# Optimization experiments

Measured on AMD Instinct MI355X. Metric: run time of the kernel, lower is better.

Reference implementation:

```python
import jax, jax.numpy as jnp
import numpy as np

B, S, E, H = 4, 2048, 1024, 16
DK = E // H  # 64


def setup_inputs() -> dict:
    key = jax.random.key(0)
    ks = jax.random.split(key, 6)
    scale = 1.0 / np.sqrt(E)
    return {
        "x": jax.random.normal(ks[0], (B, S, E), dtype=jnp.float32),
        "Wq": jax.random.normal(ks[1], (E, E), dtype=jnp.float32) * scale,
        "Wk": jax.random.normal(ks[2], (E, E), dtype=jnp.float32) * scale,
        "Wv": jax.random.normal(ks[3], (E, E), dtype=jnp.float32) * scale,
        "Wo": jax.random.normal(ks[4], (E, E), dtype=jnp.float32) * scale,
        "theta": jax.random.normal(ks[5], (DK,), dtype=jnp.float32),
    }


def _heads(t):
    # [B,S,E] -> [B,H,S,DK]
    b, s, _ = t.shape
    return t.reshape(b, s, H, DK).transpose(0, 2, 1, 3)


def reference(x, Wq, Wk, Wv, Wo, theta):
    # nn.Linear (no bias): y = x @ W.T
    # quantum transform: independent single-qubit RX(x)->RX(theta)->  <Z> = cos(x+theta)
    q = jnp.cos(_heads(x @ Wq.T) + theta)  # [B,H,S,DK]
    k = jnp.cos(_heads(x @ Wk.T) + theta)
    v = jnp.cos(_heads(x @ Wv.T) + theta)
    scores = jnp.einsum("bhqd,bhkd->bhqk", q, k) / jnp.sqrt(jnp.float32(DK))
    attn = jax.nn.softmax(scores, axis=-1)  # dropout is identity in eval
    out = jnp.einsum("bhqk,bhkd->bhqd", attn, v)  # [B,H,S,DK]
    out = out.transpose(0, 2, 1, 3).reshape(x.shape[0], -1, E)
    return out @ Wo.T
```

## Files before the change

kernel.cpp:

```cpp
#include <hip/hip_runtime.h>

#define B_  4
#define S_  2048
#define E_  1024
#define H_  16
#define DK_ 64
#define M_  (B_*S_)

typedef __attribute__((ext_vector_type(8)))  short short8;
typedef __attribute__((ext_vector_type(4)))  float f32x4;
typedef __attribute__((ext_vector_type(16))) float f32x16;

#define QSCALE 0.18033688f

__device__ __forceinline__ unsigned short f2b(float f) {
    union { float f; unsigned u; } v; v.f = f;
    unsigned u = v.u;
    return (unsigned short)((u + 0x7fffu + ((u >> 16) & 1u)) >> 16);
}

__device__ __forceinline__ void gload_lds16(const unsigned short* g, unsigned short* l) {
    __builtin_amdgcn_global_load_lds((const __attribute__((address_space(1))) void*)g,
                                     (__attribute__((address_space(3))) void*)l, 16, 0, 0);
}

#define XN4 (M_*E_/4)
#define WN4 (E_*E_/4)
__global__ __launch_bounds__(256) void cvt_all(
    const float* __restrict__ x,
    const float* __restrict__ w0, const float* __restrict__ w1,
    const float* __restrict__ w2, const float* __restrict__ w3,
    unsigned short* __restrict__ xb, unsigned short* __restrict__ wb,
    unsigned short* __restrict__ wob) {
    int i = blockIdx.x * 256 + threadIdx.x;
    const float* src;
    unsigned short* dst;
    int idx;
    if (i < XN4) { src = x; dst = xb; idx = i; }
    else {
        int j = i - XN4;
        int z = j >> 18;
        idx = j & (WN4 - 1);
        src = (z == 0) ? w0 : (z == 1) ? w1 : (z == 2) ? w2 : w3;
        dst = (z < 3) ? wb + (size_t)z * E_ * E_ : wob;
    }
    float4 f = ((const float4*)src)[idx];
    ushort4 o;
    o.x = f2b(f.x); o.y = f2b(f.y); o.z = f2b(f.z); o.w = f2b(f.w);
    ((ushort4*)dst)[idx] = o;
}

__global__ __launch_bounds__(256) void gemm_qkv(
    const unsigned short* __restrict__ xb,
    const unsigned short* __restrict__ Wb,
    const float* __restrict__ theta,
    unsigned short* __restrict__ qb,
    unsigned short* __restrict__ kb,
    unsigned short* __restrict__ vtb)
{
    __shared__ unsigned short smem[128*144];
    unsigned short* As = smem;
    unsigned short* Bs = smem + 128*64;
    const int tid = threadIdx.x;
    const int w = tid >> 6, lane = tid & 63, quad = lane >> 4, col = lane & 15;
    const int wm = (w & 1) * 64, wn = (w >> 1) * 64;
    const int m0 = blockIdx.x * 128, n0 = blockIdx.y * 128, z = blockIdx.z;
    const unsigned short* Wz = Wb + (size_t)z * E_ * E_;
    const int srow = lane >> 3;
    const int sch  = ((lane & 7) ^ srow) * 8;
    const int rsw  = col & 7;

    f32x4 acc[4][4] = {};
    for (int k0 = 0; k0 < E_; k0 += 64) {
        #pragma unroll
        for (int c = 0; c < 4; c++) {
            int row = w*32 + c*8 + srow;
            gload_lds16(&xb[(size_t)(m0+row)*E_ + k0 + sch], &As[(w*32 + c*8)*64]);
            gload_lds16(&Wz[(size_t)(n0+row)*E_ + k0 + sch], &Bs[(w*32 + c*8)*64]);
        }
        __syncthreads();
        #pragma unroll
        for (int kk = 0; kk < 64; kk += 32) {
            short8 a[4], b[4];
            #pragma unroll
            for (int i = 0; i < 4; i++)
                a[i] = *(const short8*)&As[(wm + i*16 + col)*64 + ((((kk>>3) + quad) ^ rsw) * 8)];
            #pragma unroll
            for (int j = 0; j < 4; j++)
                b[j] = *(const short8*)&Bs[(wn + j*16 + col)*64 + ((((kk>>3) + quad) ^ rsw) * 8)];
            #pragma unroll
            for (int i = 0; i < 4; i++)
                #pragma unroll
                for (int j = 0; j < 4; j++)
                    acc[i][j] = __builtin_amdgcn_mfma_f32_16x16x32_bf16(a[i], b[j], acc[i][j], 0, 0, 0);
        }
        __syncthreads();
    }

    const int bblk = m0 >> 11;
    const int sbase = m0 & (S_-1);

    if (z != 2) {
        const float qs = (z == 0) ? QSCALE : 1.0f;
        #pragma unroll
        for (int j = 0; j < 4; j++) {
            int nl = wn + j*16 + col;
            float th = theta[(n0 + nl) & 63];
            #pragma unroll
            for (int i = 0; i < 4; i++)
                #pragma unroll
                for (int r = 0; r < 4; r++) {
                    int ml = wm + i*16 + quad*4 + r;
                    int nls = nl ^ (((ml >> 2) & 3) << 4);
                    smem[ml*144 + nls] = f2b(__cosf(acc[i][j][r] + th) * qs);
                }
        }
        __syncthreads();
        unsigned short* dst = (z == 0) ? qb : kb;
        const int h0 = n0 >> 6;
        #pragma unroll
        for (int k = 0; k < 8; k++) {
            int idx = k*256 + tid;
            int chunk = idx & 7, seg = idx >> 3;
            int ml = seg >> 1, hh = seg & 1;
            int ch = chunk ^ (((ml >> 2) & 3) << 1);
            int4 val = *(const int4*)&smem[ml*144 + hh*64 + ch*8];
            size_t g = ((size_t)(bblk*H_ + h0 + hh)*S_ + sbase + ml)*DK_ + chunk*8;
            *(int4*)&dst[g] = val;
        }
    } else {
        #pragma unroll
        for (int j = 0; j < 4; j++) {
            int nl = wn + j*16 + col;
            float th = theta[(n0 + nl) & 63];
            #pragma unroll
            for (int i = 0; i < 4; i++)
                #pragma unroll
                for (int r = 0; r < 4; r++)
                    smem[nl*136 + wm + i*16 + quad*4 + r] = f2b(__cosf(acc[i][j][r] + th));
        }
        __syncthreads();
        int row = tid >> 1, halfm = (tid & 1) * 64;
        int n = n0 + row, h = n >> 6, d = n & 63;
        size_t base = ((size_t)(bblk*H_ + h)*DK_ + d)*S_ + sbase + halfm;
        #pragma unroll
        for (int k = 0; k < 8; k++)
            *(int4*)&vtb[base + k*8] = *(const int4*)&smem[row*136 + halfm + k*8];
    }
}

__global__ __launch_bounds__(256) void gemm_out(
    const unsigned short* __restrict__ ctx,
    const unsigned short* __restrict__ Wob,
    float* __restrict__ out)
{
    __shared__ unsigned short As[128*64];
    __shared__ unsigned short Bs[128*64];
    const int tid = threadIdx.x;
    const int w = tid >> 6, lane = tid & 63, quad = lane >> 4, col = lane & 15;
    const int wm = (w & 1) * 64, wn = (w >> 1) * 64;
    const int m0 = blockIdx.x * 128, n0 = blockIdx.y * 128;
    const int srow = lane >> 3;
    const int sch  = ((lane & 7) ^ srow) * 8;
    const int rsw  = col & 7;

    f32x4 acc[4][4] = {};
    for (int k0 = 0; k0 < E_; k0 += 64) {
        #pragma unroll
        for (int c = 0; c < 4; c++) {
            int row = w*32 + c*8 + srow;
            gload_lds16(&ctx[(size_t)(m0+row)*E_ + k0 + sch], &As[(w*32 + c*8)*64]);
            gload_lds16(&Wob[(size_t)(n0+row)*E_ + k0 + sch], &Bs[(w*32 + c*8)*64]);
        }
        __syncthreads();
        #pragma unroll
        for (int kk = 0; kk < 64; kk += 32) {
            short8 a[4], b[4];
            #pragma unroll
            for (int i = 0; i < 4; i++)
                a[i] = *(const short8*)&As[(wm + i*16 + col)*64 + ((((kk>>3) + quad) ^ rsw) * 8)];
            #pragma unroll
            for (int j = 0; j < 4; j++)
                b[j] = *(const short8*)&Bs[(wn + j*16 + col)*64 + ((((kk>>3) + quad) ^ rsw) * 8)];
            #pragma unroll
            for (int i = 0; i < 4; i++)
                #pragma unroll
                for (int j = 0; j < 4; j++)
                    acc[i][j] = __builtin_amdgcn_mfma_f32_16x16x32_bf16(a[i], b[j], acc[i][j], 0, 0, 0);
        }
        __syncthreads();
    }
    #pragma unroll
    for (int j = 0; j < 4; j++) {
        int n = n0 + wn + j*16 + col;
        #pragma unroll
        for (int i = 0; i < 4; i++)
            #pragma unroll
            for (int r = 0; r < 4; r++) {
                int m = m0 + wm + i*16 + quad*4 + r;
                out[(size_t)m*E_ + n] = acc[i][j][r];
            }
    }
}

#define LPK 72

__global__ __launch_bounds__(256, 4) void flash_attn(
    const unsigned short* __restrict__ qb,
    const unsigned short* __restrict__ kb,
    const unsigned short* __restrict__ vtb,
    unsigned short* __restrict__ ctx)
{
    __shared__ unsigned short Kt[2][64*LPK];
    __shared__ unsigned short Vt[2][64*LPK];
    const int tid = threadIdx.x;
    const int w = tid >> 6, lane = tid & 63, col = lane & 31, half = lane >> 5;

    const int f   = blockIdx.y * gridDim.x + blockIdx.x;
    const int swz = (f & 7) * 128 + (f >> 3);
    const int q0  = (swz & 15) * 128;
    const int bh  = swz >> 4;

    const unsigned short* kbase = kb  + (size_t)bh * S_ * DK_;
    const unsigned short* vbase = vtb + (size_t)bh * DK_ * S_;
    const int srow = tid >> 3;
    const int sc8  = (tid & 7) * 8;

    short8 qf[4];
    {
        const unsigned short* qrow = qb + ((size_t)bh*S_ + q0 + w*32 + col)*DK_;
        #pragma unroll
        for (int c = 0; c < 4; c++)
            qf[c] = *(const short8*)&qrow[c*16 + half*8];
    }

    union U8 { unsigned u[4]; short8 s8; };
    U8 ones;
    #pragma unroll
    for (int i = 0; i < 4; i++) ones.u[i] = 0x3F803F80u;

    f32x16 oacc[2] = {};
    f32x16 lacc = {};

    #pragma unroll
    for (int u = 0; u < 2; u++) {
        *(int4*)&Kt[0][(srow + u*32)*LPK + sc8] =
            *(const int4*)&kbase[(size_t)(srow + u*32)*DK_ + sc8];
        *(int4*)&Vt[0][(srow + u*32)*LPK + sc8] =
            *(const int4*)&vbase[(size_t)(srow + u*32)*S_ + sc8];
    }
    __syncthreads();

    for (int it = 0; it < S_/64; ++it) {
        const int cur = it & 1, nxt = cur ^ 1;
        const int ktn = it*64 + 64;
        int4 rk[2], rv[2];
        if (ktn < S_) {
            #pragma unroll
            for (int u = 0; u < 2; u++) {
                rk[u] = *(const int4*)&kbase[(size_t)(ktn + srow + u*32)*DK_ + sc8];
                rv[u] = *(const int4*)&vbase[(size_t)(srow + u*32)*S_ + ktn + sc8];
            }
        }

        #pragma unroll
        for (int t = 0; t < 2; t++) {
            f32x16 sacc = {};
            __builtin_amdgcn_s_setprio(1);
            #pragma unroll
            for (int c = 0; c < 4; c++) {
                short8 kf = *(const short8*)&Kt[cur][(t*32 + col)*LPK + c*16 + half*8];
                sacc = __builtin_amdgcn_mfma_f32_32x32x16_bf16(kf, qf[c], sacc, 0, 0, 0);
            }
            __builtin_amdgcn_s_setprio(0);
            unsigned pk[4][2];
            #pragma unroll
            for (int rg = 0; rg < 4; rg++) {
                float p0 = __builtin_amdgcn_exp2f(sacc[rg*4+0]);
                float p1 = __builtin_amdgcn_exp2f(sacc[rg*4+1]);
                float p2 = __builtin_amdgcn_exp2f(sacc[rg*4+2]);
                float p3 = __builtin_amdgcn_exp2f(sacc[rg*4+3]);
                pk[rg][0] = __builtin_amdgcn_perm(__float_as_uint(p1), __float_as_uint(p0), 0x07060302u);
                pk[rg][1] = __builtin_amdgcn_perm(__float_as_uint(p3), __float_as_uint(p2), 0x07060302u);
            }
            #pragma unroll
            for (int kc = 0; kc < 2; kc++) {
                const int lo = 2*kc, hi = 2*kc + 1;
                auto s0 = __builtin_amdgcn_permlane32_swap((int)pk[lo][0], (int)pk[hi][0], false, false);
                auto s1 = __builtin_amdgcn_permlane32_swap((int)pk[lo][1], (int)pk[hi][1], false, false);
                U8 pa;
                pa.u[0] = (unsigned)s0[0];
                pa.u[1] = (unsigned)s1[0];
                pa.u[2] = (unsigned)s0[1];
                pa.u[3] = (unsigned)s1[1];
                __builtin_amdgcn_s_setprio(1);
                lacc = __builtin_amdgcn_mfma_f32_32x32x16_bf16(pa.s8, ones.s8, lacc, 0, 0, 0);
                #pragma unroll
                for (int dt = 0; dt < 2; dt++) {
                    short8 vf = *(const short8*)&Vt[cur][(dt*32 + col)*LPK + t*32 + kc*16 + half*8];
                    oacc[dt] = __builtin_amdgcn_mfma_f32_32x32x16_bf16(pa.s8, vf, oacc[dt], 0, 0, 0);
                }
                __builtin_amdgcn_s_setprio(0);
            }
        }

        if (ktn < S_) {
            #pragma unroll
            for (int u = 0; u < 2; u++) {
                *(int4*)&Kt[nxt][(srow + u*32)*LPK + sc8] = rk[u];
                *(int4*)&Vt[nxt][(srow + u*32)*LPK + sc8] = rv[u];
            }
        }
        __syncthreads();
    }

    const int b = bh >> 4, h = bh & 15;
    #pragma unroll
    for (int rg = 0; rg < 4; rg++)
        #pragma unroll
        for (int rr = 0; rr < 4; rr++) {
            int row = rr + rg*8 + half*4;
            float inv = 1.0f / lacc[rg*4 + rr];
            int s = q0 + w*32 + row;
            size_t rowoff = ((size_t)(b*S_ + s))*E_ + h*64;
            #pragma unroll
            for (int dt = 0; dt < 2; dt++)
                ctx[rowoff + dt*32 + col] = f2b(oacc[dt][rg*4 + rr] * inv);
        }
}

extern "C" void kernel_launch(void* const* d_in, const int* in_sizes, int n_in,
                              void* d_out, int out_size, void* d_ws, size_t ws_size,
                              hipStream_t stream) {
    (void)in_sizes; (void)n_in; (void)out_size; (void)ws_size;
    const float* x     = (const float*)d_in[0];
    const float* Wq    = (const float*)d_in[1];
    const float* Wk    = (const float*)d_in[2];
    const float* Wv    = (const float*)d_in[3];
    const float* Wo    = (const float*)d_in[4];
    const float* theta = (const float*)d_in[5];
    float* out = (float*)d_out;

    unsigned short* ws  = (unsigned short*)d_ws;
    unsigned short* xb  = ws;
    unsigned short* Wb  = xb  + (size_t)M_*E_;
    unsigned short* Wob = Wb  + (size_t)3*E_*E_;
    unsigned short* qb  = Wob + (size_t)E_*E_;
    unsigned short* kb  = qb  + (size_t)B_*H_*S_*DK_;
    unsigned short* vtb = kb  + (size_t)B_*H_*S_*DK_;
    unsigned short* ctx = xb;

    cvt_all<<<(XN4 + 4*WN4)/256, 256, 0, stream>>>(x, Wq, Wk, Wv, Wo, xb, Wb, Wob);

    gemm_qkv<<<dim3(M_/128, E_/128, 3), 256, 0, stream>>>(xb, Wb, theta, qb, kb, vtb);
    flash_attn<<<dim3(S_/128, B_*H_), 256, 0, stream>>>(qb, kb, vtb, ctx);
    gemm_out<<<dim3(M_/128, E_/128), 256, 0, stream>>>(ctx, Wob, out);
}
```

Measured before the change: 281.9 us.

## Double query rows per warp in flash attention to reuse K/V fragments

Each warp now processes 64 query rows (two 32-row sub-tiles) instead of 32, so the block covers 256 queries and the grid halves. Each K and V fragment read from LDS now feeds two MFMAs, which halves LDS traffic and K/V global loads per query. In exchange, accumulator registers double, launch bounds drop to 2 blocks per CU, and the grid shrinks to 512 blocks, which lowers occupancy and the ability to hide latency.

```diff
diff --git a/kernel.cpp b/kernel.cpp
--- a/kernel.cpp
+++ b/kernel.cpp
@@ -205,7 +205,7 @@
 
 #define LPK 72
 
-__global__ __launch_bounds__(256, 4) void flash_attn(
+__global__ __launch_bounds__(256, 2) void flash_attn(
     const unsigned short* __restrict__ qb,
     const unsigned short* __restrict__ kb,
     const unsigned short* __restrict__ vtb,
@@ -217,21 +217,23 @@
     const int w = tid >> 6, lane = tid & 63, col = lane & 31, half = lane >> 5;
 
     const int f   = blockIdx.y * gridDim.x + blockIdx.x;
-    const int swz = (f & 7) * 128 + (f >> 3);
-    const int q0  = (swz & 15) * 128;
-    const int bh  = swz >> 4;
+    const int swz = (f & 7) * 64 + (f >> 3);
+    const int q0  = (swz & 7) * 256;
+    const int bh  = swz >> 3;
 
     const unsigned short* kbase = kb  + (size_t)bh * S_ * DK_;
     const unsigned short* vbase = vtb + (size_t)bh * DK_ * S_;
     const int srow = tid >> 3;
     const int sc8  = (tid & 7) * 8;
 
-    short8 qf[4];
+    short8 qf[2][4];
     {
-        const unsigned short* qrow = qb + ((size_t)bh*S_ + q0 + w*32 + col)*DK_;
-        #pragma unroll
-        for (int c = 0; c < 4; c++)
-            qf[c] = *(const short8*)&qrow[c*16 + half*8];
+        const unsigned short* qrow = qb + ((size_t)bh*S_ + q0 + w*64 + col)*DK_;
+        #pragma unroll
+        for (int s = 0; s < 2; s++)
+            #pragma unroll
+            for (int c = 0; c < 4; c++)
+                qf[s][c] = *(const short8*)&qrow[(size_t)s*32*DK_ + c*16 + half*8];
     }
 
     union U8 { unsigned u[4]; short8 s8; };
@@ -239,8 +241,8 @@
     #pragma unroll
     for (int i = 0; i < 4; i++) ones.u[i] = 0x3F803F80u;
 
-    f32x16 oacc[2] = {};
-    f32x16 lacc = {};
+    f32x16 oacc[2][2] = {};
+    f32x16 lacc[2] = {};
 
     #pragma unroll
     for (int u = 0; u < 2; u++) {
@@ -265,40 +267,52 @@
 
         #pragma unroll
         for (int t = 0; t < 2; t++) {
-            f32x16 sacc = {};
+            f32x16 sa0 = {}, sa1 = {};
             __builtin_amdgcn_s_setprio(1);
             #pragma unroll
             for (int c = 0; c < 4; c++) {
                 short8 kf = *(const short8*)&Kt[cur][(t*32 + col)*LPK + c*16 + half*8];
-                sacc = __builtin_amdgcn_mfma_f32_32x32x16_bf16(kf, qf[c], sacc, 0, 0, 0);
+                sa0 = __builtin_amdgcn_mfma_f32_32x32x16_bf16(kf, qf[0][c], sa0, 0, 0, 0);
+                sa1 = __builtin_amdgcn_mfma_f32_32x32x16_bf16(kf, qf[1][c], sa1, 0, 0, 0);
             }
             __builtin_amdgcn_s_setprio(0);
-            unsigned pk[4][2];
+            unsigned pk[2][4][2];
             #pragma unroll
             for (int rg = 0; rg < 4; rg++) {
-                float p0 = __builtin_amdgcn_exp2f(sacc[rg*4+0]);
-                float p1 = __builtin_amdgcn_exp2f(sacc[rg*4+1]);
-                float p2 = __builtin_amdgcn_exp2f(sacc[rg*4+2]);
-                float p3 = __builtin_amdgcn_exp2f(sacc[rg*4+3]);
-                pk[rg][0] = __builtin_amdgcn_perm(__float_as_uint(p1), __float_as_uint(p0), 0x07060302u);
-                pk[rg][1] = __builtin_amdgcn_perm(__float_as_uint(p3), __float_as_uint(p2), 0x07060302u);
+                float a0 = __builtin_amdgcn_exp2f(sa0[rg*4+0]);
+                float a1 = __builtin_amdgcn_exp2f(sa0[rg*4+1]);
+                float a2 = __builtin_amdgcn_exp2f(sa0[rg*4+2]);
+                float a3 = __builtin_amdgcn_exp2f(sa0[rg*4+3]);
+                pk[0][rg][0] = __builtin_amdgcn_perm(__float_as_uint(a1), __float_as_uint(a0), 0x07060302u);
+                pk[0][rg][1] = __builtin_amdgcn_perm(__float_as_uint(a3), __float_as_uint(a2), 0x07060302u);
+                float b0 = __builtin_amdgcn_exp2f(sa1[rg*4+0]);
+                float b1 = __builtin_amdgcn_exp2f(sa1[rg*4+1]);
+                float b2 = __builtin_amdgcn_exp2f(sa1[rg*4+2]);
+                float b3 = __builtin_amdgcn_exp2f(sa1[rg*4+3]);
+                pk[1][rg][0] = __builtin_amdgcn_perm(__float_as_uint(b1), __float_as_uint(b0), 0x07060302u);
+                pk[1][rg][1] = __builtin_amdgcn_perm(__float_as_uint(b3), __float_as_uint(b2), 0x07060302u);
             }
             #pragma unroll
             for (int kc = 0; kc < 2; kc++) {
                 const int lo = 2*kc, hi = 2*kc + 1;
-                auto s0 = __builtin_amdgcn_permlane32_swap((int)pk[lo][0], (int)pk[hi][0], false, false);
-                auto s1 = __builtin_amdgcn_permlane32_swap((int)pk[lo][1], (int)pk[hi][1], false, false);
-                U8 pa;
-                pa.u[0] = (unsigned)s0[0];
-                pa.u[1] = (unsigned)s1[0];
-                pa.u[2] = (unsigned)s0[1];
-                pa.u[3] = (unsigned)s1[1];
+                U8 pa[2];
+                #pragma unroll
+                for (int s = 0; s < 2; s++) {
+                    auto s0 = __builtin_amdgcn_permlane32_swap((int)pk[s][lo][0], (int)pk[s][hi][0], false, false);
+                    auto s1 = __builtin_amdgcn_permlane32_swap((int)pk[s][lo][1], (int)pk[s][hi][1], false, false);
+                    pa[s].u[0] = (unsigned)s0[0];
+                    pa[s].u[1] = (unsigned)s1[0];
+                    pa[s].u[2] = (unsigned)s0[1];
+                    pa[s].u[3] = (unsigned)s1[1];
+                }
                 __builtin_amdgcn_s_setprio(1);
-                lacc = __builtin_amdgcn_mfma_f32_32x32x16_bf16(pa.s8, ones.s8, lacc, 0, 0, 0);
+                lacc[0] = __builtin_amdgcn_mfma_f32_32x32x16_bf16(pa[0].s8, ones.s8, lacc[0], 0, 0, 0);
+                lacc[1] = __builtin_amdgcn_mfma_f32_32x32x16_bf16(pa[1].s8, ones.s8, lacc[1], 0, 0, 0);
                 #pragma unroll
                 for (int dt = 0; dt < 2; dt++) {
                     short8 vf = *(const short8*)&Vt[cur][(dt*32 + col)*LPK + t*32 + kc*16 + half*8];
-                    oacc[dt] = __builtin_amdgcn_mfma_f32_32x32x16_bf16(pa.s8, vf, oacc[dt], 0, 0, 0);
+                    oacc[0][dt] = __builtin_amdgcn_mfma_f32_32x32x16_bf16(pa[0].s8, vf, oacc[0][dt], 0, 0, 0);
+                    oacc[1][dt] = __builtin_amdgcn_mfma_f32_32x32x16_bf16(pa[1].s8, vf, oacc[1][dt], 0, 0, 0);
                 }
                 __builtin_amdgcn_s_setprio(0);
             }
@@ -316,17 +330,19 @@
 
     const int b = bh >> 4, h = bh & 15;
     #pragma unroll
-    for (int rg = 0; rg < 4; rg++)
-        #pragma unroll
-        for (int rr = 0; rr < 4; rr++) {
-            int row = rr + rg*8 + half*4;
-            float inv = 1.0f / lacc[rg*4 + rr];
-            int s = q0 + w*32 + row;
-            size_t rowoff = ((size_t)(b*S_ + s))*E_ + h*64;
-            #pragma unroll
-            for (int dt = 0; dt < 2; dt++)
-                ctx[rowoff + dt*32 + col] = f2b(oacc[dt][rg*4 + rr] * inv);
-        }
+    for (int s = 0; s < 2; s++)
+        #pragma unroll
+        for (int rg = 0; rg < 4; rg++)
+            #pragma unroll
+            for (int rr = 0; rr < 4; rr++) {
+                int row = rr + rg*8 + half*4;
+                float inv = 1.0f / lacc[s][rg*4 + rr];
+                int sq = q0 + w*64 + s*32 + row;
+                size_t rowoff = ((size_t)(b*S_ + sq))*E_ + h*64;
+                #pragma unroll
+                for (int dt = 0; dt < 2; dt++)
+                    ctx[rowoff + dt*32 + col] = f2b(oacc[s][dt][rg*4 + rr] * inv);
+            }
 }
 
 extern "C" void kernel_launch(void* const* d_in, const int* in_sizes, int n_in,
@@ -353,6 +369,6 @@
     cvt_all<<<(XN4 + 4*WN4)/256, 256, 0, stream>>>(x, Wq, Wk, Wv, Wo, xb, Wb, Wob);
 
     gemm_qkv<<<dim3(M_/128, E_/128, 3), 256, 0, stream>>>(xb, Wb, theta, qb, kb, vtb);
-    flash_attn<<<dim3(S_/128, B_*H_), 256, 0, stream>>>(qb, kb, vtb, ctx);
+    flash_attn<<<dim3(S_/256, B_*H_), 256, 0, stream>>>(qb, kb, vtb, ctx);
     gemm_out<<<dim3(M_/128, E_/128), 256, 0, stream>>>(ctx, Wob, out);
 }
```

Measured after the change: 260.4 us. -7.6%, faster.
